# Performance work log

Hardware: AMD Instinct MI355X
Metric: run time of the kernel (lower is better)

Reference implementation:

```python
import jax, jax.numpy as jnp
import numpy as np

BN_EPS = 1e-5
NUM_HEADS = 16


def setup_inputs() -> dict:
    key = jax.random.key(0)
    k1, k2 = jax.random.split(key)
    B, F, E = 8, 1024, 1024
    x = jax.random.normal(k1, (B, F, E), dtype=jnp.float32)
    # xavier_uniform for Linear(E, 3E): bound = sqrt(6/(E + 3E))
    bound = float(np.sqrt(6.0 / (E + 3 * E)))
    W_qkv = jax.random.uniform(k2, (3 * E, E), minval=-bound, maxval=bound, dtype=jnp.float32)
    b_qkv = jnp.zeros((3 * E,), dtype=jnp.float32)
    gamma = jnp.ones((F,), dtype=jnp.float32)
    beta = jnp.zeros((F,), dtype=jnp.float32)
    return {"x": x, "gamma": gamma, "beta": beta, "W_qkv": W_qkv, "b_qkv": b_qkv}


def reference(x, gamma, beta, W_qkv, b_qkv):
    B, F, E = x.shape
    H = NUM_HEADS
    hd = E // H
    # BatchNorm1d(features_dim) in training mode: channels = F axis,
    # stats over (batch, embed) dims, biased variance.
    mean = jnp.mean(x, axis=(0, 2), keepdims=True)          # [1,F,1]
    var = jnp.mean((x - mean) ** 2, axis=(0, 2), keepdims=True)
    xn = (x - mean) * jax.lax.rsqrt(var + BN_EPS)
    xn = xn * gamma[None, :, None] + beta[None, :, None]
    # QKV projection: torch Linear -> xn @ W^T + b
    qkv = jnp.einsum('bfe,oe->bfo', xn, W_qkv) + b_qkv       # [B,F,3E]
    qkv = qkv.reshape(B, F, H, 3 * hd).transpose(0, 2, 1, 3) # [B,H,F,3hd]
    q, k, v = jnp.split(qkv, 3, axis=-1)                     # each [B,H,F,hd]
    scale = 1.0 / jnp.sqrt(jnp.float32(hd))
    logits = jnp.einsum('bhqd,bhkd->bhqk', q, k) * scale     # [B,H,F,F]
    attn = jax.nn.softmax(logits, axis=-1)
    values = jnp.einsum('bhqk,bhkd->bhqd', attn, v)          # [B,H,F,hd]
    values = values.transpose(0, 2, 1, 3).reshape(B, F, E)
    return values
```

## Files before the change

### kernel.cpp

```cpp
#include <hip/hip_runtime.h>

typedef unsigned short u16;
typedef unsigned int   u32;

typedef __bf16 bf16x8 __attribute__((ext_vector_type(8)));
typedef float  f32x4  __attribute__((ext_vector_type(4)));

typedef const __attribute__((address_space(1))) void* gas_ptr;
typedef __attribute__((address_space(3))) void* las_ptr;

__device__ __forceinline__ u16 f2bf(float f) {
  u32 u = __builtin_bit_cast(u32, f);
  u += 0x7fffu + ((u >> 16) & 1u);
  return (u16)(u >> 16);
}
__device__ __forceinline__ float bf2f(u16 u) {
  return __builtin_bit_cast(float, ((u32)u) << 16);
}
__device__ __forceinline__ u32 cvtpk(float a, float b) {
  u32 r;
  asm("v_cvt_pk_bf16_f32 %0, %1, %2" : "=v"(r) : "v"(a), "v"(b));
  return r;
}
__device__ __forceinline__ float fexp2(float x) {
  return __builtin_amdgcn_exp2f(x);
}

__global__ __launch_bounds__(256) void bn_norm_kernel(
    const float* __restrict__ x, const float* __restrict__ gamma,
    const float* __restrict__ beta, u16* __restrict__ xn) {
  const int F = 1024, E = 1024;
  int f = blockIdx.x;
  __shared__ float sh[8192];
  __shared__ float ps[4], pq[4], sc[2];

  const float* xf = x + (size_t)f * E;
  float ls = 0.f, lq = 0.f;
  for (int i = threadIdx.x; i < 8192; i += 256) {
    int b = i >> 10, e = i & 1023;
    float v = xf[(size_t)b * F * E + e];
    sh[i] = v;
    ls += v;
    lq += v * v;
  }
  #pragma unroll
  for (int o = 32; o > 0; o >>= 1) {
    ls += __shfl_down(ls, o, 64);
    lq += __shfl_down(lq, o, 64);
  }
  int w = threadIdx.x >> 6;
  if ((threadIdx.x & 63) == 0) { ps[w] = ls; pq[w] = lq; }
  __syncthreads();
  if (threadIdx.x == 0) {
    float s = ps[0] + ps[1] + ps[2] + ps[3];
    float q = pq[0] + pq[1] + pq[2] + pq[3];
    float mean = s * (1.f / 8192.f);
    float var = q * (1.f / 8192.f) - mean * mean;
    float scale = gamma[f] * rsqrtf(var + 1e-5f);
    sc[0] = scale;
    sc[1] = beta[f] - mean * scale;
  }
  __syncthreads();
  float scale = sc[0], shift = sc[1];
  for (int i = threadIdx.x; i < 8192; i += 256) {
    int b = i >> 10, e = i & 1023;
    xn[((size_t)(b * F + f)) * E + e] = f2bf(sh[i] * scale + shift);
  }
}

__global__ __launch_bounds__(256) void wconv_kernel(
    const float* __restrict__ W, u16* __restrict__ Wb) {
  const int total = 3072 * 1024 / 4;
  for (int i = blockIdx.x * 256 + threadIdx.x; i < total; i += gridDim.x * 256) {
    float4 v = ((const float4*)W)[i];
    ushort4 o;
    o.x = f2bf(v.x); o.y = f2bf(v.y); o.z = f2bf(v.z); o.w = f2bf(v.w);
    ((ushort4*)Wb)[i] = o;
  }
}

__global__ __launch_bounds__(256) void gemm_qkv_kernel(
    const u16* __restrict__ A, const u16* __restrict__ Bw,
    const float* __restrict__ bias, u16* __restrict__ C,
    u16* __restrict__ Vt) {
  const int K = 1024, N = 3072;
  __shared__ u16 As[128 * 32];
  __shared__ u16 Bs[128 * 32];

  int m0 = blockIdx.x * 128, n0 = blockIdx.y * 128;
  int t = threadIdx.x, lane = t & 63, w = t >> 6;
  int wr = w >> 1, wc = w & 1;
  int r = lane & 15, g = lane >> 4;

  int srow = t >> 2;
  int scol = ((t & 3) ^ ((srow >> 1) & 3)) * 8;
  const u16* gA  = A  + (size_t)(m0 + srow) * K + scol;
  const u16* gA2 = A  + (size_t)(m0 + 64 + srow) * K + scol;
  const u16* gB  = Bw + (size_t)(n0 + srow) * K + scol;
  const u16* gB2 = Bw + (size_t)(n0 + 64 + srow) * K + scol;
  u16* lA  = As + t * 8;
  u16* lA2 = As + 2048 + t * 8;
  u16* lB  = Bs + t * 8;
  u16* lB2 = Bs + 2048 + t * 8;

  f32x4 acc[4][4] = {};

  int rc = (g ^ ((r >> 1) & 3)) * 8;
  const u16* pA = As + (size_t)(wr * 64 + r) * 32 + rc;
  const u16* pB = Bs + (size_t)(wc * 64 + r) * 32 + rc;

  for (int k0 = 0; k0 < K; k0 += 32) {
    __builtin_amdgcn_global_load_lds((gas_ptr)gA,  (las_ptr)lA,  16, 0, 0);
    __builtin_amdgcn_global_load_lds((gas_ptr)gA2, (las_ptr)lA2, 16, 0, 0);
    __builtin_amdgcn_global_load_lds((gas_ptr)gB,  (las_ptr)lB,  16, 0, 0);
    __builtin_amdgcn_global_load_lds((gas_ptr)gB2, (las_ptr)lB2, 16, 0, 0);
    gA += 32; gA2 += 32; gB += 32; gB2 += 32;
    __syncthreads();

    bf16x8 af[4], bfr[4];
    #pragma unroll
    for (int mi = 0; mi < 4; ++mi)
      af[mi] = __builtin_bit_cast(bf16x8, *(const int4*)(pA + mi * 512));
    #pragma unroll
    for (int ni = 0; ni < 4; ++ni)
      bfr[ni] = __builtin_bit_cast(bf16x8, *(const int4*)(pB + ni * 512));
    #pragma unroll
    for (int mi = 0; mi < 4; ++mi)
      #pragma unroll
      for (int ni = 0; ni < 4; ++ni)
        acc[mi][ni] = __builtin_amdgcn_mfma_f32_16x16x32_bf16(af[mi], bfr[ni], acc[mi][ni], 0, 0, 0);
    __syncthreads();
  }

  int b_ = m0 >> 10;
  #pragma unroll
  for (int ni = 0; ni < 4; ++ni) {
    int colb = n0 + wc * 64 + ni * 16;
    int col = colb + r;
    float bv = bias[col];
    int h_ = colb / 192;
    int rr = colb - h_ * 192;
    if (rr >= 128) {
      int d_ = rr - 128 + r;
      u16* vtd = Vt + (size_t)(b_ * 16 + h_) * 65536 + (size_t)d_ * 1024;
      #pragma unroll
      for (int mi = 0; mi < 4; ++mi) {
        int fbase = (m0 & 1023) + wr * 64 + mi * 16 + g * 4;
        int pos = (fbase & ~31) + ((g >> 1) * 16) + ((g & 1) * 8) + ((mi & 1) * 4);
        uint2 st;
        st.x = cvtpk(acc[mi][ni][0] + bv, acc[mi][ni][1] + bv);
        st.y = cvtpk(acc[mi][ni][2] + bv, acc[mi][ni][3] + bv);
        *(uint2*)(vtd + pos) = st;
      }
    } else {
      #pragma unroll
      for (int mi = 0; mi < 4; ++mi) {
        int row = m0 + wr * 64 + mi * 16 + g * 4;
        #pragma unroll
        for (int j = 0; j < 4; ++j)
          C[(size_t)(row + j) * N + col] = f2bf(acc[mi][ni][j] + bv);
      }
    }
  }
}

__global__ __launch_bounds__(256) void attn_kernel(
    const u16* __restrict__ qkv, const u16* __restrict__ Vt,
    float* __restrict__ out) {
  const int F = 1024, NQ = 3072;
  int bid = blockIdx.x;
  int xcd = bid & 7;
  int li  = bid >> 3;
  int bh  = ((li >> 4) << 3) | xcd;
  int ql  = li & 15;
  int w   = threadIdx.x >> 6;
  int lane = threadIdx.x & 63;
  int q = lane & 15, g = lane >> 4;
  int qs = q & 7;
  int q0 = ql * 64 + w * 16;
  int b = bh >> 4, h = bh & 15;

  const u16* base = qkv + (size_t)b * F * NQ + h * 192;
  const u16* VtBH = Vt + (size_t)bh * 65536;

  __shared__ u16 S[24576];

  int i8 = lane >> 3;
  int ic = lane & 7;

  const float qscale = 0.125f * 1.4426950408889634f;
  bf16x8 Qf0, Qf1;
  {
    const u16* qp = base + (size_t)(q0 + q) * NQ + g * 8;
    union { int4 v; u16 u[8]; } uu0, uu1;
    uu0.v = *(const int4*)(qp);
    uu1.v = *(const int4*)(qp + 32);
    union { u32 w4[4]; bf16x8 v; } p0, p1;
    #pragma unroll
    for (int j = 0; j < 4; ++j) {
      p0.w4[j] = cvtpk(bf2f(uu0.u[2 * j]) * qscale, bf2f(uu0.u[2 * j + 1]) * qscale);
      p1.w4[j] = cvtpk(bf2f(uu1.u[2 * j]) * qscale, bf2f(uu1.u[2 * j + 1]) * qscale);
    }
    Qf0 = p0.v; Qf1 = p1.v;
  }

  f32x4 acc[4] = {};
  float m = 0.0f, lsum = 0.f;

  #define STAGE(buf, kt)                                                       \
    do {                                                                       \
      int kb_ = (kt) * 64;                                                     \
      _Pragma("unroll")                                                        \
      for (int rr = 0; rr < 2; ++rr) {                                         \
        int r_ = rr * 32 + w * 8 + i8;                                         \
        int sc_ = (ic ^ (r_ & 7)) * 8;                                         \
        const u16* ks_ = base + (size_t)(kb_ + r_) * NQ + 64 + sc_;            \
        const u16* vs_ = VtBH + (size_t)r_ * 1024 + kb_ + sc_;                 \
        __builtin_amdgcn_global_load_lds((gas_ptr)ks_,                         \
            (las_ptr)&S[(buf) * 4096 + (rr * 32 + w * 8) * 64], 16, 0, 0);     \
        __builtin_amdgcn_global_load_lds((gas_ptr)vs_,                         \
            (las_ptr)&S[12288 + (buf) * 4096 + (rr * 32 + w * 8) * 64], 16, 0, 0);\
      }                                                                        \
    } while (0)

  __builtin_amdgcn_sched_barrier(0);
  STAGE(0, 0);
  STAGE(1, 1);
  asm volatile("s_waitcnt vmcnt(4)" ::: "memory");
  __builtin_amdgcn_s_barrier();
  __builtin_amdgcn_sched_barrier(0);

  #pragma unroll
  for (int kt = 0; kt < 16; ++kt) {
    const int cur = kt % 3;
    const int stg = (kt + 2) % 3;
    if (kt < 14) STAGE(stg, kt + 2);

    const u16* Kb = &S[cur * 4096];
    const u16* Vb = &S[12288 + cur * 4096];

    f32x4 s[4];
    f32x4 seed = {-m, -m, -m, -m};
    __builtin_amdgcn_s_setprio(1);
    #pragma unroll
    for (int ks = 0; ks < 4; ++ks) {
      int row = ks * 16 + q;
      int4 k0 = *(const int4*)&Kb[row * 64 + ((g ^ qs) * 8)];
      int4 k1 = *(const int4*)&Kb[row * 64 + (((4 + g) ^ qs) * 8)];
      f32x4 sv = seed;
      sv = __builtin_amdgcn_mfma_f32_16x16x32_bf16(__builtin_bit_cast(bf16x8, k0), Qf0, sv, 0, 0, 0);
      sv = __builtin_amdgcn_mfma_f32_16x16x32_bf16(__builtin_bit_cast(bf16x8, k1), Qf1, sv, 0, 0, 0);
      s[ks] = sv;
    }
    __builtin_amdgcn_s_setprio(0);

    float a0 = fmaxf(fmaxf(s[0][0], s[0][1]), s[0][2]);
    float a1 = fmaxf(fmaxf(s[0][3], s[1][0]), s[1][1]);
    float a2 = fmaxf(fmaxf(s[1][2], s[1][3]), s[2][0]);
    float a3 = fmaxf(fmaxf(s[2][1], s[2][2]), s[2][3]);
    float a4 = fmaxf(fmaxf(s[3][0], s[3][1]), s[3][2]);
    float tmx = fmaxf(fmaxf(fmaxf(a0, a1), a2), fmaxf(fmaxf(a3, a4), s[3][3]));

    float p[16];
    if (__builtin_expect(__any(tmx > 8.0f), 0)) {
      float tr = fmaxf(tmx, __shfl_xor(tmx, 16, 64));
      tr = fmaxf(tr, __shfl_xor(tr, 32, 64));
      float dm = fmaxf(tr, 0.f);
      float alpha = fexp2(-dm);
      lsum *= alpha;
      acc[0] *= alpha; acc[1] *= alpha; acc[2] *= alpha; acc[3] *= alpha;
      m += dm;
      #pragma unroll
      for (int ks = 0; ks < 4; ++ks) {
        p[ks * 4 + 0] = fexp2(s[ks][0] - dm);
        p[ks * 4 + 1] = fexp2(s[ks][1] - dm);
        p[ks * 4 + 2] = fexp2(s[ks][2] - dm);
        p[ks * 4 + 3] = fexp2(s[ks][3] - dm);
      }
    } else {
      #pragma unroll
      for (int ks = 0; ks < 4; ++ks) {
        p[ks * 4 + 0] = fexp2(s[ks][0]);
        p[ks * 4 + 1] = fexp2(s[ks][1]);
        p[ks * 4 + 2] = fexp2(s[ks][2]);
        p[ks * 4 + 3] = fexp2(s[ks][3]);
      }
    }
    float q01 = p[0] + p[1],   q23 = p[2] + p[3];
    float q45 = p[4] + p[5],   q67 = p[6] + p[7];
    float q89 = p[8] + p[9],   qab = p[10] + p[11];
    float qcd = p[12] + p[13], qef = p[14] + p[15];
    lsum += ((q01 + q23) + (q45 + q67)) + ((q89 + qab) + (qcd + qef));

    union { u32 w4[4]; bf16x8 v; } pb0, pb1;
    pb0.w4[0] = cvtpk(p[0], p[1]);   pb0.w4[1] = cvtpk(p[2], p[3]);
    pb0.w4[2] = cvtpk(p[4], p[5]);   pb0.w4[3] = cvtpk(p[6], p[7]);
    pb1.w4[0] = cvtpk(p[8], p[9]);   pb1.w4[1] = cvtpk(p[10], p[11]);
    pb1.w4[2] = cvtpk(p[12], p[13]); pb1.w4[3] = cvtpk(p[14], p[15]);

    __builtin_amdgcn_s_setprio(1);
    #pragma unroll
    for (int dt = 0; dt < 4; ++dt) {
      int row = dt * 16 + q;
      int4 v0 = *(const int4*)&Vb[row * 64 + ((g ^ qs) * 8)];
      int4 v1 = *(const int4*)&Vb[row * 64 + (((4 + g) ^ qs) * 8)];
      acc[dt] = __builtin_amdgcn_mfma_f32_16x16x32_bf16(__builtin_bit_cast(bf16x8, v0), pb0.v, acc[dt], 0, 0, 0);
      acc[dt] = __builtin_amdgcn_mfma_f32_16x16x32_bf16(__builtin_bit_cast(bf16x8, v1), pb1.v, acc[dt], 0, 0, 0);
    }
    __builtin_amdgcn_s_setprio(0);

    if (kt < 14) {
      asm volatile("s_waitcnt vmcnt(4)" ::: "memory");
    } else {
      asm volatile("s_waitcnt vmcnt(0)" ::: "memory");
    }
    __builtin_amdgcn_s_barrier();
    __builtin_amdgcn_sched_barrier(0);
  }
  #undef STAGE

  lsum += __shfl_xor(lsum, 16, 64);
  lsum += __shfl_xor(lsum, 32, 64);
  float inv = 1.0f / lsum;

  float* oT = (float*)S + (size_t)w * 1088;
  #pragma unroll
  for (int dt = 0; dt < 4; ++dt) {
    oT[(dt * 16 + g * 4 + 0) * 17 + q] = acc[dt][0] * inv;
    oT[(dt * 16 + g * 4 + 1) * 17 + q] = acc[dt][1] * inv;
    oT[(dt * 16 + g * 4 + 2) * 17 + q] = acc[dt][2] * inv;
    oT[(dt * 16 + g * 4 + 3) * 17 + q] = acc[dt][3] * inv;
  }
  asm volatile("s_waitcnt lgkmcnt(0)" ::: "memory");
  int oq = lane >> 2, dc = (lane & 3) * 16;
  float* orow = out + (size_t)(b * F + q0 + oq) * 1024 + h * 64 + dc;
  #pragma unroll
  for (int c4 = 0; c4 < 4; ++c4) {
    float4 v;
    v.x = oT[(dc + c4 * 4 + 0) * 17 + oq];
    v.y = oT[(dc + c4 * 4 + 1) * 17 + oq];
    v.z = oT[(dc + c4 * 4 + 2) * 17 + oq];
    v.w = oT[(dc + c4 * 4 + 3) * 17 + oq];
    *(float4*)(orow + c4 * 4) = v;
  }
}

extern "C" void kernel_launch(void* const* d_in, const int* in_sizes, int n_in,
                              void* d_out, int out_size, void* d_ws, size_t ws_size,
                              hipStream_t stream) {
  const float* x     = (const float*)d_in[0];
  const float* gamma = (const float*)d_in[1];
  const float* beta  = (const float*)d_in[2];
  const float* W     = (const float*)d_in[3];
  const float* bias  = (const float*)d_in[4];
  float* out = (float*)d_out;

  char* ws = (char*)d_ws;
  u16* xn  = (u16*)ws;
  u16* Wb  = (u16*)(ws + (size_t)16 * 1024 * 1024);
  u16* qkv = (u16*)(ws + (size_t)22 * 1024 * 1024);
  u16* Vt  = (u16*)(ws + (size_t)70 * 1024 * 1024);

  bn_norm_kernel<<<1024, 256, 0, stream>>>(x, gamma, beta, xn);
  wconv_kernel<<<768, 256, 0, stream>>>(W, Wb);
  gemm_qkv_kernel<<<dim3(64, 24), 256, 0, stream>>>(xn, Wb, bias, qkv, Vt);
  attn_kernel<<<2048, 256, 0, stream>>>(qkv, Vt, out);
}
```

Before: 144.4 us.

## Use 128-key tiles with double buffering and compute row sums via MFMA

The attention kernel now processes 128 keys per iteration instead of 64, with two LDS buffers instead of three. The V tile layout is widened to 128 columns with a 16-way XOR swizzle. The softmax denominator now comes from an MFMA against a ones vector, which replaces the scalar adds and cross-lane shuffles. This halves loop iterations and barriers but cuts the prefetch depth and raises register pressure from 32 probabilities. It also adds four extra MFMAs per tile and sums the bf16-rounded probabilities rather than the fp32 ones.

```diff
diff --git a/kernel.cpp b/kernel.cpp
--- a/kernel.cpp
+++ b/kernel.cpp
@@ -183,7 +183,7 @@
   const u16* base = qkv + (size_t)b * F * NQ + h * 192;
   const u16* VtBH = Vt + (size_t)bh * 65536;
 
-  __shared__ u16 S[24576];
+  __shared__ u16 S[32768];
 
   int i8 = lane >> 3;
   int ic = lane & 7;
@@ -204,46 +204,56 @@
     Qf0 = p0.v; Qf1 = p1.v;
   }
 
+  union { u16 u[8]; bf16x8 v; } ones_;
+  #pragma unroll
+  for (int j = 0; j < 8; ++j) ones_.u[j] = 0x3F80;
+  const bf16x8 Ones = ones_.v;
+
   f32x4 acc[4] = {};
-  float m = 0.0f, lsum = 0.f;
+  f32x4 accS = {};
+  float m = 0.0f;
 
   #define STAGE(buf, kt)                                                       \
     do {                                                                       \
-      int kb_ = (kt) * 64;                                                     \
+      int kb_ = (kt) * 128;                                                    \
       _Pragma("unroll")                                                        \
-      for (int rr = 0; rr < 2; ++rr) {                                         \
+      for (int rr = 0; rr < 4; ++rr) {                                         \
         int r_ = rr * 32 + w * 8 + i8;                                         \
         int sc_ = (ic ^ (r_ & 7)) * 8;                                         \
         const u16* ks_ = base + (size_t)(kb_ + r_) * NQ + 64 + sc_;            \
-        const u16* vs_ = VtBH + (size_t)r_ * 1024 + kb_ + sc_;                 \
         __builtin_amdgcn_global_load_lds((gas_ptr)ks_,                         \
-            (las_ptr)&S[(buf) * 4096 + (rr * 32 + w * 8) * 64], 16, 0, 0);     \
+            (las_ptr)&S[(buf) * 8192 + (rr * 32 + w * 8) * 64], 16, 0, 0);     \
+      }                                                                        \
+      _Pragma("unroll")                                                        \
+      for (int jj = 0; jj < 4; ++jj) {                                         \
+        int slot = jj * 256 + w * 64 + lane;                                   \
+        int vr_ = slot >> 4;                                                   \
+        int vc_ = slot & 15;                                                   \
+        int sc_ = (vc_ ^ (vr_ & 15)) * 8;                                      \
+        const u16* vs_ = VtBH + (size_t)vr_ * 1024 + kb_ + sc_;                \
         __builtin_amdgcn_global_load_lds((gas_ptr)vs_,                         \
-            (las_ptr)&S[12288 + (buf) * 4096 + (rr * 32 + w * 8) * 64], 16, 0, 0);\
+            (las_ptr)&S[16384 + (buf) * 8192 + (jj * 256 + w * 64) * 8], 16, 0, 0);\
       }                                                                        \
     } while (0)
 
-  __builtin_amdgcn_sched_barrier(0);
   STAGE(0, 0);
-  STAGE(1, 1);
-  asm volatile("s_waitcnt vmcnt(4)" ::: "memory");
+  asm volatile("s_waitcnt vmcnt(0)" ::: "memory");
   __builtin_amdgcn_s_barrier();
   __builtin_amdgcn_sched_barrier(0);
 
   #pragma unroll
-  for (int kt = 0; kt < 16; ++kt) {
-    const int cur = kt % 3;
-    const int stg = (kt + 2) % 3;
-    if (kt < 14) STAGE(stg, kt + 2);
-
-    const u16* Kb = &S[cur * 4096];
-    const u16* Vb = &S[12288 + cur * 4096];
-
-    f32x4 s[4];
+  for (int kt = 0; kt < 8; ++kt) {
+    const int cur = kt & 1;
+    if (kt < 7) STAGE(cur ^ 1, kt + 1);
+
+    const u16* Kb = &S[cur * 8192];
+    const u16* Vb = &S[16384 + cur * 8192];
+
+    f32x4 s[8];
     f32x4 seed = {-m, -m, -m, -m};
     __builtin_amdgcn_s_setprio(1);
     #pragma unroll
-    for (int ks = 0; ks < 4; ++ks) {
+    for (int ks = 0; ks < 8; ++ks) {
       int row = ks * 16 + q;
       int4 k0 = *(const int4*)&Kb[row * 64 + ((g ^ qs) * 8)];
       int4 k1 = *(const int4*)&Kb[row * 64 + (((4 + g) ^ qs) * 8)];
@@ -254,24 +264,24 @@
     }
     __builtin_amdgcn_s_setprio(0);
 
-    float a0 = fmaxf(fmaxf(s[0][0], s[0][1]), s[0][2]);
-    float a1 = fmaxf(fmaxf(s[0][3], s[1][0]), s[1][1]);
-    float a2 = fmaxf(fmaxf(s[1][2], s[1][3]), s[2][0]);
-    float a3 = fmaxf(fmaxf(s[2][1], s[2][2]), s[2][3]);
-    float a4 = fmaxf(fmaxf(s[3][0], s[3][1]), s[3][2]);
-    float tmx = fmaxf(fmaxf(fmaxf(a0, a1), a2), fmaxf(fmaxf(a3, a4), s[3][3]));
-
-    float p[16];
+    float mk[8];
+    #pragma unroll
+    for (int ks = 0; ks < 8; ++ks)
+      mk[ks] = fmaxf(fmaxf(s[ks][0], s[ks][1]), fmaxf(s[ks][2], s[ks][3]));
+    float tmx = fmaxf(fmaxf(fmaxf(mk[0], mk[1]), fmaxf(mk[2], mk[3])),
+                      fmaxf(fmaxf(mk[4], mk[5]), fmaxf(mk[6], mk[7])));
+
+    float p[32];
     if (__builtin_expect(__any(tmx > 8.0f), 0)) {
       float tr = fmaxf(tmx, __shfl_xor(tmx, 16, 64));
       tr = fmaxf(tr, __shfl_xor(tr, 32, 64));
       float dm = fmaxf(tr, 0.f);
       float alpha = fexp2(-dm);
-      lsum *= alpha;
       acc[0] *= alpha; acc[1] *= alpha; acc[2] *= alpha; acc[3] *= alpha;
+      accS *= alpha;
       m += dm;
       #pragma unroll
-      for (int ks = 0; ks < 4; ++ks) {
+      for (int ks = 0; ks < 8; ++ks) {
         p[ks * 4 + 0] = fexp2(s[ks][0] - dm);
         p[ks * 4 + 1] = fexp2(s[ks][1] - dm);
         p[ks * 4 + 2] = fexp2(s[ks][2] - dm);
@@ -279,49 +289,46 @@
       }
     } else {
       #pragma unroll
-      for (int ks = 0; ks < 4; ++ks) {
+      for (int ks = 0; ks < 8; ++ks) {
         p[ks * 4 + 0] = fexp2(s[ks][0]);
         p[ks * 4 + 1] = fexp2(s[ks][1]);
         p[ks * 4 + 2] = fexp2(s[ks][2]);
         p[ks * 4 + 3] = fexp2(s[ks][3]);
       }
     }
-    float q01 = p[0] + p[1],   q23 = p[2] + p[3];
-    float q45 = p[4] + p[5],   q67 = p[6] + p[7];
-    float q89 = p[8] + p[9],   qab = p[10] + p[11];
-    float qcd = p[12] + p[13], qef = p[14] + p[15];
-    lsum += ((q01 + q23) + (q45 + q67)) + ((q89 + qab) + (qcd + qef));
-
-    union { u32 w4[4]; bf16x8 v; } pb0, pb1;
-    pb0.w4[0] = cvtpk(p[0], p[1]);   pb0.w4[1] = cvtpk(p[2], p[3]);
-    pb0.w4[2] = cvtpk(p[4], p[5]);   pb0.w4[3] = cvtpk(p[6], p[7]);
-    pb1.w4[0] = cvtpk(p[8], p[9]);   pb1.w4[1] = cvtpk(p[10], p[11]);
-    pb1.w4[2] = cvtpk(p[12], p[13]); pb1.w4[3] = cvtpk(p[14], p[15]);
+
+    union { u32 w4[4]; bf16x8 v; } pb[4];
+    #pragma unroll
+    for (int cc = 0; cc < 4; ++cc) {
+      pb[cc].w4[0] = cvtpk(p[cc * 8 + 0], p[cc * 8 + 1]);
+      pb[cc].w4[1] = cvtpk(p[cc * 8 + 2], p[cc * 8 + 3]);
+      pb[cc].w4[2] = cvtpk(p[cc * 8 + 4], p[cc * 8 + 5]);
+      pb[cc].w4[3] = cvtpk(p[cc * 8 + 6], p[cc * 8 + 7]);
+    }
 
     __builtin_amdgcn_s_setprio(1);
     #pragma unroll
     for (int dt = 0; dt < 4; ++dt) {
       int row = dt * 16 + q;
-      int4 v0 = *(const int4*)&Vb[row * 64 + ((g ^ qs) * 8)];
-      int4 v1 = *(const int4*)&Vb[row * 64 + (((4 + g) ^ qs) * 8)];
-      acc[dt] = __builtin_amdgcn_mfma_f32_16x16x32_bf16(__builtin_bit_cast(bf16x8, v0), pb0.v, acc[dt], 0, 0, 0);
-      acc[dt] = __builtin_amdgcn_mfma_f32_16x16x32_bf16(__builtin_bit_cast(bf16x8, v1), pb1.v, acc[dt], 0, 0, 0);
-    }
+      #pragma unroll
+      for (int cc = 0; cc < 4; ++cc) {
+        int4 vv = *(const int4*)&Vb[row * 128 + (((cc * 4 + g) ^ q) * 8)];
+        acc[dt] = __builtin_amdgcn_mfma_f32_16x16x32_bf16(
+            __builtin_bit_cast(bf16x8, vv), pb[cc].v, acc[dt], 0, 0, 0);
+      }
+    }
+    #pragma unroll
+    for (int cc = 0; cc < 4; ++cc)
+      accS = __builtin_amdgcn_mfma_f32_16x16x32_bf16(Ones, pb[cc].v, accS, 0, 0, 0);
     __builtin_amdgcn_s_setprio(0);
 
-    if (kt < 14) {
-      asm volatile("s_waitcnt vmcnt(4)" ::: "memory");
-    } else {
-      asm volatile("s_waitcnt vmcnt(0)" ::: "memory");
-    }
+    asm volatile("s_waitcnt vmcnt(0)" ::: "memory");
     __builtin_amdgcn_s_barrier();
     __builtin_amdgcn_sched_barrier(0);
   }
   #undef STAGE
 
-  lsum += __shfl_xor(lsum, 16, 64);
-  lsum += __shfl_xor(lsum, 32, 64);
-  float inv = 1.0f / lsum;
+  float inv = 1.0f / accS[0];
 
   float* oT = (float*)S + (size_t)w * 1088;
   #pragma unroll
```

After: 150.2 us. 4.0% more time.
